# Kernel optimization log

Hardware: AMD Instinct MI355X
Metric: run time of the kernel (lower is better)

Reference implementation:

```python
import jax, jax.numpy as jnp
import numpy as np

N_HEAD = 16
D_HEAD = 64
D_MODEL = 1024
B, T = 2, 2048


def setup_inputs() -> dict:
    key = jax.random.key(0)
    ks = jax.random.split(key, 5)
    s = 1.0 / np.sqrt(D_MODEL)
    return {
        "x": jax.random.normal(ks[0], (B, T, D_MODEL), dtype=jnp.float32),
        "wq": jax.random.normal(ks[1], (D_MODEL, D_MODEL), dtype=jnp.float32) * s,
        "wk": jax.random.normal(ks[2], (D_MODEL, D_MODEL), dtype=jnp.float32) * s,
        "wv": jax.random.normal(ks[3], (D_MODEL, D_MODEL), dtype=jnp.float32) * s,
        "wo": jax.random.normal(ks[4], (D_MODEL, D_MODEL), dtype=jnp.float32) * s,
    }


def reference(x, wq, wk, wv, wo):
    Bb, Tt, D = x.shape
    H, Dh = N_HEAD, D_HEAD
    # Linear projections (flax Linear: y = x @ kernel), split heads
    q = (x @ wq).reshape(Bb, Tt, H, Dh)
    k = (x @ wk).reshape(Bb, Tt, H, Dh)
    v = (x @ wv).reshape(Bb, Tt, H, Dh)
    scale = jnp.sqrt(jnp.asarray(Dh)).astype(x.dtype)
    scores = jnp.einsum('bthd,bshd->bhts', q, k) / scale  # [B,H,T,T]
    mask = jnp.tril(jnp.ones((Tt, Tt), dtype=jnp.bool_))
    scores = jnp.where(mask, scores, jnp.finfo(scores.dtype).min)
    attn = jax.nn.softmax(scores, axis=-1)
    out = jnp.einsum('bhts,bshd->bthd', attn, v).reshape(Bb, Tt, D)
    return out @ wo
```

## Files before the change

kernel.cpp:

```cpp
#include <hip/hip_runtime.h>
#include <math.h>

#define DEV static __device__ __forceinline__

typedef __attribute__((ext_vector_type(4))) float f32x4;
typedef __attribute__((ext_vector_type(2))) unsigned u32x2;
typedef __attribute__((ext_vector_type(8))) __bf16 bf16x8;
typedef __attribute__((ext_vector_type(8))) unsigned short u16x8;
typedef __attribute__((ext_vector_type(4))) unsigned short u16x4;

constexpr int TB = 2;
constexpr int TT = 2048;
constexpr int DM = 1024;
constexpr int NH = 16;
constexpr int DH = 64;
constexpr int MR = TB * TT;
constexpr int SQKV = 3 * DM;

DEV unsigned short f2bf(float f) {
  union { float f; unsigned u; } v; v.f = f;
  return (unsigned short)((v.u + 0x7FFFu + ((v.u >> 16) & 1u)) >> 16);
}

DEV unsigned cvtpk(float a, float b) {
  unsigned r;
  asm("v_cvt_pk_bf16_f32 %0, %1, %2" : "=v"(r) : "v"(a), "v"(b));
  return r;
}

DEV void gld16(const void* g, void* l) {
  __builtin_amdgcn_global_load_lds((const __attribute__((address_space(1))) void*)g,
                                   (__attribute__((address_space(3))) void*)l, 16, 0, 0);
}

DEV bf16x8 ldsb8(const unsigned short* p) { return *(const bf16x8*)p; }

__global__ __launch_bounds__(256) void k_prep(const float* __restrict__ x,
                                              const float* __restrict__ w0,
                                              const float* __restrict__ w1,
                                              const float* __restrict__ w2,
                                              const float* __restrict__ w3,
                                              unsigned short* __restrict__ xb,
                                              unsigned short* __restrict__ wtdst) {
  __shared__ float tile[32][33];
  const int id = blockIdx.x, tid = threadIdx.x;
  if (id < 4096) {
    const int z = id >> 10, tl = id & 1023;
    const float* w = z == 0 ? w0 : z == 1 ? w1 : z == 2 ? w2 : w3;
    unsigned short* wt = wtdst + (size_t)z * DM * DM;
    const int n0 = (tl & 31) * 32, k0 = (tl >> 5) * 32;
    const int tx = tid & 31, ty = tid >> 5;
#pragma unroll
    for (int yy = 0; yy < 32; yy += 8)
      tile[ty + yy][tx] = w[(size_t)(k0 + ty + yy) * DM + n0 + tx];
    __syncthreads();
#pragma unroll
    for (int yy = 0; yy < 32; yy += 8)
      wt[(size_t)(n0 + ty + yy) * DM + k0 + tx] = f2bf(tile[tx][ty + yy]);
  } else {
    const int i = ((id - 4096) * 256 + tid) * 8;
    f32x4 a = *(const f32x4*)(x + i);
    f32x4 b = *(const f32x4*)(x + i + 4);
    u16x8 o;
#pragma unroll
    for (int j = 0; j < 4; ++j) { o[j] = f2bf(a[j]); o[j + 4] = f2bf(b[j]); }
    *(u16x8*)(xb + i) = o;
  }
}

DEV void store_c(float* p, float v) { *p = v; }
DEV void store_c(unsigned short* p, float v) { *p = f2bf(v); }

__global__ __launch_bounds__(512) void k_gemm_qkv(const unsigned short* __restrict__ A,
                                                  const unsigned short* __restrict__ Bt,
                                                  unsigned short* __restrict__ C,
                                                  float ascale,
                                                  unsigned short* __restrict__ vt) {
  constexpr int K = DM, N = SQKV, NS = K / 32;
  __shared__ alignas(16) unsigned short As[2][128 * 32];
  __shared__ alignas(16) unsigned short Bs[2][128 * 32];
  const int tid = threadIdx.x;
  const int m0 = blockIdx.y * 128, n0 = blockIdx.x * 128;
  const int lane = tid & 63, w = tid >> 6;
  const int lr = lane & 15, lg = lane >> 4;
  const int wm = w >> 2, wn = w & 3;
  const int srow = tid >> 2, scc = (tid & 3) ^ ((srow >> 1) & 3);
  const unsigned short* Ab = A + (size_t)(m0 + srow) * K + scc * 8;
  const unsigned short* Bb = Bt + (size_t)(n0 + srow) * K + scc * 8;
  auto stage = [&](int buf, int s) {
    gld16(Ab + s * 32, (void*)(As[buf] + tid * 8));
    gld16(Bb + s * 32, (void*)(Bs[buf] + tid * 8));
  };
  f32x4 acc[4][2] = {};
  stage(0, 0);
  for (int s = 0; s < NS; ++s) {
    const int buf = s & 1;
    asm volatile("s_waitcnt vmcnt(0)" ::: "memory");
    __builtin_amdgcn_s_barrier();
    if (s + 1 < NS) stage(buf ^ 1, s + 1);
    bf16x8 af[4], bfr[2];
#pragma unroll
    for (int i = 0; i < 4; ++i) {
      const int row = wm * 64 + i * 16 + lr;
      af[i] = ldsb8(As[buf] + row * 32 + ((lg ^ ((row >> 1) & 3)) * 8));
    }
#pragma unroll
    for (int j = 0; j < 2; ++j) {
      const int row = wn * 32 + j * 16 + lr;
      bfr[j] = ldsb8(Bs[buf] + row * 32 + ((lg ^ ((row >> 1) & 3)) * 8));
    }
    __builtin_amdgcn_s_setprio(1);
#pragma unroll
    for (int i = 0; i < 4; ++i)
#pragma unroll
      for (int j = 0; j < 2; ++j)
        acc[i][j] = __builtin_amdgcn_mfma_f32_16x16x32_bf16(af[i], bfr[j], acc[i][j], 0, 0, 0);
    __builtin_amdgcn_s_setprio(0);
  }
#pragma unroll
  for (int i = 0; i < 4; ++i)
#pragma unroll
    for (int j = 0; j < 2; ++j) {
      const int row = m0 + wm * 64 + i * 16 + lg * 4;
      const int col = n0 + wn * 32 + j * 16 + lr;
      if (col >= 2 * DM) {
        const int hh = (col - 2 * DM) >> 6, dd = (col - 2 * DM) & 63;
        const int bb = row >> 11, sg = row & (TT - 1);
        const int t = sg >> 6, sl = sg & 63;
        const int g = ((sl >> 5) << 2) | ((sl >> 2) & 3);
        const int half = (sl >> 4) & 1;
        const int cch = g ^ (dd & 7);
        u16x4 pk;
#pragma unroll
        for (int r = 0; r < 4; ++r) pk[r] = f2bf(acc[i][j][r]);
        *(u16x4*)(vt + (size_t)((bb * NH + hh) * 32 + t) * 4096 + dd * 64 + cch * 8 + half * 4) = pk;
      } else {
        const float s = (col < DM) ? ascale : 1.0f;
#pragma unroll
        for (int r = 0; r < 4; ++r)
          store_c(C + (size_t)(row + r) * N + col, acc[i][j][r] * s);
      }
    }
}

__global__ __launch_bounds__(512) void k_gemm_out(const unsigned short* __restrict__ A,
                                                  const unsigned short* __restrict__ Bt,
                                                  float* __restrict__ C) {
  constexpr int K = DM, N = DM, NS = K / 32;
  __shared__ alignas(16) unsigned short As[2][128 * 32];
  __shared__ alignas(16) unsigned short Bs[2][64 * 32];
  const int tid = threadIdx.x;
  const int m0 = blockIdx.y * 128, n0 = blockIdx.x * 64;
  const int lane = tid & 63, w = tid >> 6;
  const int lr = lane & 15, lg = lane >> 4;
  const int wm = w >> 1, wn = w & 1;
  const int srow = tid >> 2, scc = (tid & 3) ^ ((srow >> 1) & 3);
  const unsigned short* Ab = A + (size_t)(m0 + srow) * K + scc * 8;
  const unsigned short* Bb = (tid < 256) ? Bt + (size_t)(n0 + srow) * K + scc * 8 : nullptr;
  auto stage = [&](int buf, int s) {
    gld16(Ab + s * 32, (void*)(As[buf] + tid * 8));
    if (tid < 256) gld16(Bb + s * 32, (void*)(Bs[buf] + tid * 8));
  };
  f32x4 acc[2][2] = {};
  stage(0, 0);
  for (int s = 0; s < NS; ++s) {
    const int buf = s & 1;
    asm volatile("s_waitcnt vmcnt(0)" ::: "memory");
    __builtin_amdgcn_s_barrier();
    if (s + 1 < NS) stage(buf ^ 1, s + 1);
    bf16x8 af[2], bfr[2];
#pragma unroll
    for (int i = 0; i < 2; ++i) {
      const int row = wm * 32 + i * 16 + lr;
      af[i] = ldsb8(As[buf] + row * 32 + ((lg ^ ((row >> 1) & 3)) * 8));
    }
#pragma unroll
    for (int j = 0; j < 2; ++j) {
      const int row = wn * 32 + j * 16 + lr;
      bfr[j] = ldsb8(Bs[buf] + row * 32 + ((lg ^ ((row >> 1) & 3)) * 8));
    }
    __builtin_amdgcn_s_setprio(1);
#pragma unroll
    for (int i = 0; i < 2; ++i)
#pragma unroll
      for (int j = 0; j < 2; ++j)
        acc[i][j] = __builtin_amdgcn_mfma_f32_16x16x32_bf16(af[i], bfr[j], acc[i][j], 0, 0, 0);
    __builtin_amdgcn_s_setprio(0);
  }
#pragma unroll
  for (int i = 0; i < 2; ++i)
#pragma unroll
    for (int j = 0; j < 2; ++j) {
      const int row = m0 + wm * 32 + i * 16 + lg * 4;
      const int col = n0 + wn * 32 + j * 16 + lr;
#pragma unroll
      for (int r = 0; r < 4; ++r) C[(size_t)(row + r) * N + col] = acc[i][j][r];
    }
}

__global__ __launch_bounds__(512) void k_attn12(const unsigned short* __restrict__ QKV,
                                                const unsigned short* __restrict__ Vt,
                                                unsigned short* __restrict__ O) {
  __shared__ alignas(16) unsigned short Ks[3][64 * 64];
  __shared__ alignas(16) unsigned short Vs[3][64 * 64];
  const int id = blockIdx.x;
  const int pairIdx = id & 255;
  const int bh = pairIdx >> 3, pi = pairIdx & 7;
  const int j = (id < 256) ? pi : 15 - pi;
  const int b = bh >> 4, h = bh & 15;
  const int q0 = j * 128;
  const int tid = threadIdx.x, lane = tid & 63, w = tid >> 6;
  const int lr = lane & 15, lg = lane >> 4;
  const int lsw = lr & 7;
  const int qw = q0 + w * 16;
  const unsigned short* Qg = QKV + (size_t)b * TT * SQKV + h * DH;
  const unsigned short* Kg = QKV + (size_t)b * TT * SQKV + DM + h * DH;
  const unsigned short* Vg = Vt + (size_t)bh * 32 * 4096;

  bf16x8 qf[2];
#pragma unroll
  for (int c2 = 0; c2 < 2; ++c2)
    qf[c2] = *(const bf16x8*)(Qg + (size_t)(qw + lr) * SQKV + c2 * 32 + lg * 8);

  f32x4 acco[4] = {};
  float lrun = 0.f;

  const int krow = tid >> 3, kcc = (tid & 7) ^ (krow & 7);
  const unsigned short* kbase = Kg + (size_t)krow * SQKV + kcc * 8;
  const unsigned short* vbase = Vg + tid * 8;
  auto stage = [&](int buf, int t) {
    gld16(kbase + (size_t)t * 64 * SQKV, (void*)(Ks[buf] + tid * 8));
    gld16(vbase + (size_t)t * 4096, (void*)(Vs[buf] + tid * 8));
  };

  const int nt = 2 * j + 2;
  stage(0, 0);
  stage(1, 1);
  int buf = 0;
  for (int t = 0; t < nt; ++t) {
    if (t + 1 < nt) {
      asm volatile("s_waitcnt vmcnt(2)" ::: "memory");
    } else {
      asm volatile("s_waitcnt vmcnt(0)" ::: "memory");
    }
    __builtin_amdgcn_s_barrier();
    if (t + 2 < nt) {
      int nb = buf + 2; if (nb >= 3) nb -= 3;
      stage(nb, t + 2);
    }
    const int s0 = t * 64;
    if (s0 <= qw + 15) {
      const unsigned short* Kb_ = Ks[buf];
      const unsigned short* Vb_ = Vs[buf];
      f32x4 st[4] = {};
      __builtin_amdgcn_s_setprio(1);
#pragma unroll
      for (int ct = 0; ct < 4; ++ct)
#pragma unroll
        for (int c2 = 0; c2 < 2; ++c2) {
          bf16x8 kf = ldsb8(Kb_ + (ct * 16 + lr) * 64 + (((c2 * 4 + lg) ^ lsw) * 8));
          st[ct] = __builtin_amdgcn_mfma_f32_16x16x32_bf16(kf, qf[c2], st[ct], 0, 0, 0);
        }
      __builtin_amdgcn_s_setprio(0);
      float p[4][4];
      const int qrel = qw + lr - s0;
      if (s0 + 63 >= qw) {
#pragma unroll
        for (int ct = 0; ct < 4; ++ct)
#pragma unroll
          for (int r = 0; r < 4; ++r) {
            float v = st[ct][r];
            if (ct * 16 + lg * 4 + r > qrel) v = -1e30f;
            p[ct][r] = v;
          }
      } else {
#pragma unroll
        for (int ct = 0; ct < 4; ++ct)
#pragma unroll
          for (int r = 0; r < 4; ++r) p[ct][r] = st[ct][r];
      }
      f32x4 rs4 = {0.f, 0.f, 0.f, 0.f};
#pragma unroll
      for (int ct = 0; ct < 4; ++ct)
#pragma unroll
        for (int r = 0; r < 4; ++r) {
          p[ct][r] = __builtin_exp2f(p[ct][r]);
          rs4[r] += p[ct][r];
        }
      float rs = (rs4[0] + rs4[1]) + (rs4[2] + rs4[3]);
      rs += __shfl_xor(rs, 16);
      rs += __shfl_xor(rs, 32);
      lrun += rs;
      bf16x8 pf[2];
#pragma unroll
      for (int ks = 0; ks < 2; ++ks) {
        union { unsigned w4[4]; bf16x8 v; } pu;
        pu.w4[0] = cvtpk(p[2 * ks][0], p[2 * ks][1]);
        pu.w4[1] = cvtpk(p[2 * ks][2], p[2 * ks][3]);
        pu.w4[2] = cvtpk(p[2 * ks + 1][0], p[2 * ks + 1][1]);
        pu.w4[3] = cvtpk(p[2 * ks + 1][2], p[2 * ks + 1][3]);
        pf[ks] = pu.v;
      }
      __builtin_amdgcn_s_setprio(1);
#pragma unroll
      for (int dt = 0; dt < 4; ++dt) {
        const unsigned short* Vrow = Vb_ + (dt * 16 + lr) * 64;
#pragma unroll
        for (int ks = 0; ks < 2; ++ks) {
          bf16x8 vf = ldsb8(Vrow + (((ks * 4 + lg) ^ lsw) * 8));
          acco[dt] = __builtin_amdgcn_mfma_f32_16x16x32_bf16(pf[ks], vf, acco[dt], 0, 0, 0);
        }
      }
      __builtin_amdgcn_s_setprio(0);
    }
    if (++buf >= 3) buf = 0;
  }
  const float linv = 1.f / lrun;
  float lb[4];
#pragma unroll
  for (int r = 0; r < 4; ++r) lb[r] = __shfl(linv, lg * 4 + r);
#pragma unroll
  for (int dt = 0; dt < 4; ++dt)
#pragma unroll
    for (int r = 0; r < 4; ++r) {
      const int q = qw + lg * 4 + r;
      O[(size_t)(b * TT + q) * DM + h * DH + dt * 16 + lr] = f2bf(acco[dt][r] * lb[r]);
    }
}

extern "C" void kernel_launch(void* const* d_in, const int* in_sizes, int n_in,
                              void* d_out, int out_size, void* d_ws, size_t ws_size,
                              hipStream_t stream) {
  const float* x = (const float*)d_in[0];
  const float* wq = (const float*)d_in[1];
  const float* wk = (const float*)d_in[2];
  const float* wv = (const float*)d_in[3];
  const float* wo = (const float*)d_in[4];
  float* out = (float*)d_out;
  char* ws = (char*)d_ws;
  const size_t MB = 1u << 20;
  unsigned short* xb = (unsigned short*)(ws);
  unsigned short* wqt = (unsigned short*)(ws + 8 * MB);
  unsigned short* wot = (unsigned short*)(ws + 14 * MB);
  unsigned short* QKVb = (unsigned short*)(ws + 16 * MB);
  unsigned short* Vtb = (unsigned short*)(ws + 40 * MB);

  k_prep<<<dim3(6144), 256, 0, stream>>>(x, wq, wk, wv, wo, xb, wqt);
  k_gemm_qkv<<<dim3(24, 32), 512, 0, stream>>>(xb, wqt, QKVb, 0.18033688f, Vtb);
  k_attn12<<<dim3(512), 512, 0, stream>>>(QKVb, Vtb, xb);
  k_gemm_out<<<dim3(16, 32), 512, 0, stream>>>(xb, wot, out);
}
```

Before: 113.8 us.

## Split long causal query tiles across two blocks and pre-swizzle K layout

The QKV GEMM now writes Q separately and stores K in a pre-swizzled per-head tile layout, so attention loads K with contiguous 16-byte loads. The attention grid grows to 768 blocks using a static schedule table: heavy query tiles (j>=8) have their KV range split into two halves whose unnormalized partial outputs and row sums go to fp32 scratch. A new normalization kernel merges them, which balances the causal workload across CUs. The cost is an extra kernel launch and extra fp32 scratch traffic, and the merge relies on both halves sharing a fixed max rather than a running one.

```diff
diff --git a/kernel.cpp b/kernel.cpp
--- a/kernel.cpp
+++ b/kernel.cpp
@@ -68,15 +68,13 @@
   }
 }
 
-DEV void store_c(float* p, float v) { *p = v; }
-DEV void store_c(unsigned short* p, float v) { *p = f2bf(v); }
-
 __global__ __launch_bounds__(512) void k_gemm_qkv(const unsigned short* __restrict__ A,
                                                   const unsigned short* __restrict__ Bt,
-                                                  unsigned short* __restrict__ C,
+                                                  unsigned short* __restrict__ Qb,
                                                   float ascale,
+                                                  unsigned short* __restrict__ kp,
                                                   unsigned short* __restrict__ vt) {
-  constexpr int K = DM, N = SQKV, NS = K / 32;
+  constexpr int K = DM, NS = K / 32;
   __shared__ alignas(16) unsigned short As[2][128 * 32];
   __shared__ alignas(16) unsigned short Bs[2][128 * 32];
   const int tid = threadIdx.x;
@@ -123,22 +121,29 @@
     for (int j = 0; j < 2; ++j) {
       const int row = m0 + wm * 64 + i * 16 + lg * 4;
       const int col = n0 + wn * 32 + j * 16 + lr;
-      if (col >= 2 * DM) {
+      const int bb = row >> 11, sg = row & (TT - 1);
+      if (col < DM) {
+#pragma unroll
+        for (int r = 0; r < 4; ++r)
+          Qb[(size_t)(row + r) * DM + col] = f2bf(acc[i][j][r] * ascale);
+      } else if (col < 2 * DM) {
+        const int hh = (col - DM) >> 6, dd = (col - DM) & 63;
+        unsigned short* kb = kp + (size_t)(bb * NH + hh) * 32 * 4096;
+#pragma unroll
+        for (int r = 0; r < 4; ++r) {
+          const int s = sg + r, t = s >> 6, sl = s & 63;
+          kb[t * 4096 + sl * 64 + (((dd >> 3) ^ (sl & 7)) * 8) + (dd & 7)] = f2bf(acc[i][j][r]);
+        }
+      } else {
         const int hh = (col - 2 * DM) >> 6, dd = (col - 2 * DM) & 63;
-        const int bb = row >> 11, sg = row & (TT - 1);
         const int t = sg >> 6, sl = sg & 63;
         const int g = ((sl >> 5) << 2) | ((sl >> 2) & 3);
-        const int half = (sl >> 4) & 1;
+        const int hf2 = (sl >> 4) & 1;
         const int cch = g ^ (dd & 7);
         u16x4 pk;
 #pragma unroll
         for (int r = 0; r < 4; ++r) pk[r] = f2bf(acc[i][j][r]);
-        *(u16x4*)(vt + (size_t)((bb * NH + hh) * 32 + t) * 4096 + dd * 64 + cch * 8 + half * 4) = pk;
-      } else {
-        const float s = (col < DM) ? ascale : 1.0f;
-#pragma unroll
-        for (int r = 0; r < 4; ++r)
-          store_c(C + (size_t)(row + r) * N + col, acc[i][j][r] * s);
+        *(u16x4*)(vt + (size_t)((bb * NH + hh) * 32 + t) * 4096 + dd * 64 + cch * 8 + hf2 * 4) = pk;
       }
     }
 }
@@ -198,53 +203,60 @@
     }
 }
 
-__global__ __launch_bounds__(512) void k_attn12(const unsigned short* __restrict__ QKV,
+__constant__ const signed char JV[24]  = {15,7,14,14,13,13,12,11, 15,6,12,10,10,9,11,5, 0,1,2,3,8,4,8,9};
+__constant__ const signed char T0v[24] = {0,0,0,15,0,14,13,12, 16,0,0,0,11,0,0,0, 0,0,0,0,0,0,9,10};
+__constant__ const signed char CNTv[24]= {16,16,15,15,14,14,13,12, 16,14,13,11,11,10,12,12, 2,4,6,8,9,10,9,10};
+
+__global__ __launch_bounds__(512) void k_attn13(const unsigned short* __restrict__ Qb,
+                                                const unsigned short* __restrict__ Kp,
                                                 const unsigned short* __restrict__ Vt,
-                                                unsigned short* __restrict__ O) {
+                                                unsigned short* __restrict__ O,
+                                                float* __restrict__ Oacc0,
+                                                float* __restrict__ Oacc1,
+                                                float* __restrict__ lacc0,
+                                                float* __restrict__ lacc1) {
   __shared__ alignas(16) unsigned short Ks[3][64 * 64];
   __shared__ alignas(16) unsigned short Vs[3][64 * 64];
   const int id = blockIdx.x;
-  const int pairIdx = id & 255;
-  const int bh = pairIdx >> 3, pi = pairIdx & 7;
-  const int j = (id < 256) ? pi : 15 - pi;
+  const int rank = id >> 5, bh = id & 31;
+  const int j = JV[rank], t0 = T0v[rank], cnt = CNTv[rank];
+  const bool split = (j >= 8);
+  const int hf = (t0 > 0) ? 1 : 0;
   const int b = bh >> 4, h = bh & 15;
   const int q0 = j * 128;
   const int tid = threadIdx.x, lane = tid & 63, w = tid >> 6;
   const int lr = lane & 15, lg = lane >> 4;
   const int lsw = lr & 7;
   const int qw = q0 + w * 16;
-  const unsigned short* Qg = QKV + (size_t)b * TT * SQKV + h * DH;
-  const unsigned short* Kg = QKV + (size_t)b * TT * SQKV + DM + h * DH;
-  const unsigned short* Vg = Vt + (size_t)bh * 32 * 4096;
+  const unsigned short* Qg = Qb + (size_t)b * TT * DM + h * DH;
+  const unsigned short* kbase = Kp + (size_t)bh * 32 * 4096 + tid * 8;
+  const unsigned short* vbase = Vt + (size_t)bh * 32 * 4096 + tid * 8;
 
   bf16x8 qf[2];
 #pragma unroll
   for (int c2 = 0; c2 < 2; ++c2)
-    qf[c2] = *(const bf16x8*)(Qg + (size_t)(qw + lr) * SQKV + c2 * 32 + lg * 8);
+    qf[c2] = *(const bf16x8*)(Qg + (size_t)(qw + lr) * DM + c2 * 32 + lg * 8);
 
   f32x4 acco[4] = {};
   float lrun = 0.f;
 
-  const int krow = tid >> 3, kcc = (tid & 7) ^ (krow & 7);
-  const unsigned short* kbase = Kg + (size_t)krow * SQKV + kcc * 8;
-  const unsigned short* vbase = Vg + tid * 8;
   auto stage = [&](int buf, int t) {
-    gld16(kbase + (size_t)t * 64 * SQKV, (void*)(Ks[buf] + tid * 8));
+    gld16(kbase + (size_t)t * 4096, (void*)(Ks[buf] + tid * 8));
     gld16(vbase + (size_t)t * 4096, (void*)(Vs[buf] + tid * 8));
   };
 
-  const int nt = 2 * j + 2;
-  stage(0, 0);
-  stage(1, 1);
+  stage(0, t0);
+  stage(1, t0 + 1);
   int buf = 0;
-  for (int t = 0; t < nt; ++t) {
-    if (t + 1 < nt) {
+  for (int k = 0; k < cnt; ++k) {
+    const int t = t0 + k;
+    if (k + 1 < cnt) {
       asm volatile("s_waitcnt vmcnt(2)" ::: "memory");
     } else {
       asm volatile("s_waitcnt vmcnt(0)" ::: "memory");
     }
     __builtin_amdgcn_s_barrier();
-    if (t + 2 < nt) {
+    if (k + 2 < cnt) {
       int nb = buf + 2; if (nb >= 3) nb -= 3;
       stage(nb, t + 2);
     }
@@ -315,17 +327,55 @@
     }
     if (++buf >= 3) buf = 0;
   }
-  const float linv = 1.f / lrun;
-  float lb[4];
-#pragma unroll
-  for (int r = 0; r < 4; ++r) lb[r] = __shfl(linv, lg * 4 + r);
-#pragma unroll
-  for (int dt = 0; dt < 4; ++dt)
-#pragma unroll
-    for (int r = 0; r < 4; ++r) {
-      const int q = qw + lg * 4 + r;
-      O[(size_t)(b * TT + q) * DM + h * DH + dt * 16 + lr] = f2bf(acco[dt][r] * lb[r]);
-    }
+  if (!split) {
+    const float linv = 1.f / lrun;
+    float lb[4];
+#pragma unroll
+    for (int r = 0; r < 4; ++r) lb[r] = __shfl(linv, lg * 4 + r);
+#pragma unroll
+    for (int dt = 0; dt < 4; ++dt)
+#pragma unroll
+      for (int r = 0; r < 4; ++r) {
+        const int q = qw + lg * 4 + r;
+        O[(size_t)(b * TT + q) * DM + h * DH + dt * 16 + lr] = f2bf(acco[dt][r] * lb[r]);
+      }
+  } else {
+    const int jj = j - 8;
+    float* Oa = (hf ? Oacc1 : Oacc0) + (size_t)(bh * 8 + jj) * 128 * 64;
+    float* la = (hf ? lacc1 : lacc0) + (size_t)(bh * 8 + jj) * 128;
+#pragma unroll
+    for (int dt = 0; dt < 4; ++dt)
+#pragma unroll
+      for (int r = 0; r < 4; ++r)
+        Oa[(w * 16 + lg * 4 + r) * 64 + dt * 16 + lr] = acco[dt][r];
+    if (lg == 0) la[w * 16 + lr] = lrun;
+  }
+}
+
+__global__ __launch_bounds__(256) void k_norm(const float* __restrict__ Oacc0,
+                                              const float* __restrict__ Oacc1,
+                                              const float* __restrict__ lacc0,
+                                              const float* __restrict__ lacc1,
+                                              unsigned short* __restrict__ O) {
+  const int gid = blockIdx.x * 256 + threadIdx.x;
+  const int f = gid * 8;
+  const int d0 = f & 63, row = (f >> 6) & 127, jj = (f >> 13) & 7, bh = f >> 16;
+  const int b = bh >> 4, h = bh & 15;
+  const size_t ri = (size_t)(bh * 8 + jj) * 128 + row;
+  const size_t oi = ri * 64 + d0;
+  f32x4 a0 = *(const f32x4*)(Oacc0 + oi);
+  f32x4 a1 = *(const f32x4*)(Oacc0 + oi + 4);
+  f32x4 b0 = *(const f32x4*)(Oacc1 + oi);
+  f32x4 b1 = *(const f32x4*)(Oacc1 + oi + 4);
+  const float linv = 1.f / (lacc0[ri] + lacc1[ri]);
+  u16x8 o;
+#pragma unroll
+  for (int r = 0; r < 4; ++r) {
+    o[r] = f2bf((a0[r] + b0[r]) * linv);
+    o[r + 4] = f2bf((a1[r] + b1[r]) * linv);
+  }
+  const int q = 1024 + jj * 128 + row;
+  *(u16x8*)(O + (size_t)(b * TT + q) * DM + h * DH + d0) = o;
 }
 
 extern "C" void kernel_launch(void* const* d_in, const int* in_sizes, int n_in,
@@ -340,13 +390,19 @@
   char* ws = (char*)d_ws;
   const size_t MB = 1u << 20;
   unsigned short* xb = (unsigned short*)(ws);
+  float* Oacc0 = (float*)(ws);
   unsigned short* wqt = (unsigned short*)(ws + 8 * MB);
+  float* lacc0 = (float*)(ws + 8 * MB);
+  float* lacc1 = (float*)(ws + 8 * MB + (32 * 8 * 128) * 4);
   unsigned short* wot = (unsigned short*)(ws + 14 * MB);
-  unsigned short* QKVb = (unsigned short*)(ws + 16 * MB);
-  unsigned short* Vtb = (unsigned short*)(ws + 40 * MB);
+  unsigned short* Qb = (unsigned short*)(ws + 16 * MB);
+  unsigned short* Kp = (unsigned short*)(ws + 24 * MB);
+  unsigned short* Vtb = (unsigned short*)(ws + 32 * MB);
+  float* Oacc1 = (float*)(ws + 40 * MB);
 
   k_prep<<<dim3(6144), 256, 0, stream>>>(x, wq, wk, wv, wo, xb, wqt);
-  k_gemm_qkv<<<dim3(24, 32), 512, 0, stream>>>(xb, wqt, QKVb, 0.18033688f, Vtb);
-  k_attn12<<<dim3(512), 512, 0, stream>>>(QKVb, Vtb, xb);
-  k_gemm_out<<<dim3(16, 32), 512, 0, stream>>>(xb, wot, out);
-}
+  k_gemm_qkv<<<dim3(24, 32), 512, 0, stream>>>(xb, wqt, Qb, 0.18033688f, Kp, Vtb);
+  k_attn13<<<dim3(768), 512, 0, stream>>>(Qb, Kp, Vtb, Qb, Oacc0, Oacc1, lacc0, lacc1);
+  k_norm<<<dim3(1024), 256, 0, stream>>>(Oacc0, Oacc1, lacc0, lacc1, Qb);
+  k_gemm_out<<<dim3(16, 32), 512, 0, stream>>>(Qb, wot, out);
+}
```

Result: faster. 106.4 us (-6.5%).
